# Optimization experiments

Measured on AMD Instinct MI355X. Metric: run time of the kernel, lower is better.

The kernel has to match this reference:

```python
import jax, jax.numpy as jnp
import numpy as np

N_HEAD = 16


def setup_inputs() -> dict:
    key = jax.random.key(0)
    k1, k2, k3 = jax.random.split(key, 3)
    B, T, N = 4, 2048, 1024
    x = jax.random.normal(k1, (B, T, N), dtype=jnp.float32)
    W_attn = jax.random.normal(k2, (N, 3 * N), dtype=jnp.float32) * (1.0 / np.sqrt(N))
    b_attn = jnp.zeros((3 * N,), dtype=jnp.float32)
    W_proj = jax.random.normal(k3, (N, N), dtype=jnp.float32) * (1.0 / np.sqrt(N))
    b_proj = jnp.zeros((N,), dtype=jnp.float32)
    return {"x": x, "W_attn": W_attn, "b_attn": b_attn, "W_proj": W_proj, "b_proj": b_proj}


def reference(x, W_attn, b_attn, W_proj, b_proj):
    B, T, N = x.shape
    H = N_HEAD
    Dh = N // H
    qkv = x @ W_attn + b_attn                      # [B, T, 3N]
    q, k, v = jnp.split(qkv, 3, axis=2)
    # [B, H, T, Dh]
    q = q.reshape(B, T, H, Dh).transpose(0, 2, 1, 3)
    k = k.reshape(B, T, H, Dh).transpose(0, 2, 1, 3)
    v = v.reshape(B, T, H, Dh).transpose(0, 2, 1, 3)
    att = jnp.einsum('bhqd,bhkd->bhqk', q, k) / (Dh ** 0.5)
    mask = jnp.tril(jnp.ones((T, T), dtype=bool))
    att = jnp.where(mask[None, None], att, jnp.finfo(x.dtype).min)
    att = jax.nn.softmax(att, axis=-1)
    y = jnp.einsum('bhqk,bhkd->bhqd', att, v)      # [B, H, T, Dh]
    y = y.transpose(0, 2, 1, 3).reshape(B, T, N)
    return y @ W_proj + b_proj
```

## Files before the change

kernel.cpp:

```cpp
#include <hip/hip_runtime.h>
#include <hip/hip_bf16.h>


typedef __attribute__((ext_vector_type(8))) short short8;
typedef __attribute__((ext_vector_type(4))) float f32x4;
typedef __attribute__((ext_vector_type(16))) float f32x16;

#define MFMA16(a, b, c) __builtin_amdgcn_mfma_f32_16x16x32_bf16((a), (b), (c), 0, 0, 0)
#define MFMA32(a, b, c) __builtin_amdgcn_mfma_f32_32x32x16_bf16((a), (b), (c), 0, 0, 0)

#if defined(__has_builtin)
#if __has_builtin(__builtin_amdgcn_exp2f)
#define EXP2(x) __builtin_amdgcn_exp2f(x)
#endif
#endif
#ifndef EXP2
#define EXP2(x) exp2f(x)
#endif

__device__ __forceinline__ void gload_lds16(const void* g, void* l) {
  __builtin_amdgcn_global_load_lds(
      (const __attribute__((address_space(1))) unsigned int*)g,
      (__attribute__((address_space(3))) unsigned int*)l, 16, 0, 0);
}

__device__ __forceinline__ unsigned pack_bf16x2(float lo, float hi) {
  unsigned ulo = __float_as_uint(lo) + 0x8000u;
  unsigned uhi = __float_as_uint(hi) + 0x8000u;
  return __builtin_amdgcn_perm(uhi, ulo, 0x07060302u);
}

__device__ __forceinline__ unsigned short bf16u(float f) {
  return (unsigned short)((__float_as_uint(f) + 0x8000u) >> 16);
}

__global__ void prep_kernel(const float* __restrict__ x, unsigned* __restrict__ Xb,
                            const float* __restrict__ Wa, __hip_bfloat16* __restrict__ WaT,
                            const float* __restrict__ Wp, __hip_bfloat16* __restrict__ WpT) {
  __shared__ float tile[32][33];
  const int tid = threadIdx.x;
  int blk = blockIdx.x;
  if (blk >= 4096) {
    int i = (blk - 4096) * 256 + tid;
    float4 v = ((const float4*)x)[i];
    uint2 o;
    o.x = pack_bf16x2(v.x, v.y);
    o.y = pack_bf16x2(v.z, v.w);
    ((uint2*)Xb)[i] = o;
    return;
  }
  const float* src;
  __hip_bfloat16* dst;
  int R, C, bx, by;
  if (blk < 3072) {
    src = Wa; dst = WaT; R = 1024; C = 3072; bx = blk % 96; by = blk / 96;
  } else {
    blk -= 3072;
    src = Wp; dst = WpT; R = 1024; C = 1024; bx = blk & 31; by = blk >> 5;
  }
  const int tx = tid & 31, ty = tid >> 5;
  const int c0 = bx * 32, r0 = by * 32;
#pragma unroll
  for (int i = 0; i < 32; i += 8)
    tile[ty + i][tx] = src[(long)(r0 + ty + i) * C + c0 + tx];
  __syncthreads();
#pragma unroll
  for (int i = 0; i < 32; i += 8)
    dst[(long)(c0 + ty + i) * R + r0 + tx] = __float2bfloat16(tile[tx][ty + i]);
}

template <int EPI>
__global__ __launch_bounds__(256, 2) void gemm_bt(
    const __hip_bfloat16* __restrict__ A, const __hip_bfloat16* __restrict__ Bt,
    const float* __restrict__ bias, void* o0, void* o1, void* o2, int N, int K) {
  __shared__ alignas(16) char smem[34816];
  short8 (*As)[8] = (short8(*)[8])smem;
  short8 (*Bs)[8] = (short8(*)[8])(smem + 16384);
  unsigned short (*C16)[136] = (unsigned short(*)[136])smem;
  float (*C32)[132] = (float(*)[132])smem;

  const int tid = threadIdx.x;
  const int lane = tid & 63, w = tid >> 6;
  const int l15 = lane & 15, quad = lane >> 4;
  const int wm = (w >> 1) * 64, wn = (w & 1) * 64;
  const int rowBase = blockIdx.y * 128;
  const int colBase = blockIdx.x * 128;
  const int sr8 = lane >> 3;
  const int scc = (lane & 7) ^ sr8;

  f32x4 acc[4][4];
#pragma unroll
  for (int mi = 0; mi < 4; ++mi)
#pragma unroll
    for (int ni = 0; ni < 4; ++ni)
      acc[mi][ni] = {0.f, 0.f, 0.f, 0.f};

  for (int k0 = 0; k0 < K; k0 += 64) {
    __syncthreads();
#pragma unroll
    for (int p = 0; p < 4; ++p) {
      const int rb = p * 32 + w * 8;
      const int row = rb + sr8;
      gload_lds16(A + (rowBase + row) * K + k0 + scc * 8, &As[rb][0]);
      gload_lds16(Bt + (colBase + row) * K + k0 + scc * 8, &Bs[rb][0]);
    }
    __syncthreads();
#pragma unroll
    for (int kc = 0; kc < 2; ++kc) {
      short8 af[4], bf[4];
#pragma unroll
      for (int mi = 0; mi < 4; ++mi) {
        int row = wm + mi * 16 + l15;
        af[mi] = As[row][(kc * 4 + quad) ^ (row & 7)];
      }
#pragma unroll
      for (int ni = 0; ni < 4; ++ni) {
        int row = wn + ni * 16 + l15;
        bf[ni] = Bs[row][(kc * 4 + quad) ^ (row & 7)];
      }
#pragma unroll
      for (int mi = 0; mi < 4; ++mi)
#pragma unroll
        for (int ni = 0; ni < 4; ++ni)
          acc[mi][ni] = MFMA16(af[mi], bf[ni], acc[mi][ni]);
    }
  }

  float bcol[4];
#pragma unroll
  for (int ni = 0; ni < 4; ++ni) bcol[ni] = bias[colBase + wn + ni * 16 + l15];

  if (EPI == 0) {
    const int which = colBase >> 10;
    const int b = rowBase >> 11;
    const int tt0 = rowBase & 2047;
    const int n1base = colBase & 1023;
    const float osc = (which == 0) ? 0.180336880111f : 1.0f;
    __syncthreads();
    if (which != 2) {
#pragma unroll
      for (int mi = 0; mi < 4; ++mi)
#pragma unroll
        for (int ni = 0; ni < 4; ++ni)
#pragma unroll
          for (int r = 0; r < 4; ++r)
            C16[wm + mi * 16 + quad * 4 + r][wn + ni * 16 + l15] =
                bf16u((acc[mi][ni][r] + bcol[ni]) * osc);
    } else {
#pragma unroll
      for (int mi = 0; mi < 4; ++mi)
#pragma unroll
        for (int ni = 0; ni < 4; ++ni)
#pragma unroll
          for (int r = 0; r < 4; ++r)
            C16[wn + ni * 16 + l15][wm + mi * 16 + quad * 4 + r] =
                bf16u(acc[mi][ni][r] + bcol[ni]);
    }
    __syncthreads();
    unsigned short* o = (unsigned short*)(which == 0 ? o0 : which == 1 ? o1 : o2);
    if (which != 2) {
#pragma unroll
      for (int j = 0; j < 8; ++j) {
        int flat = j * 256 + tid;
        int trow = flat >> 4, ch = flat & 15;
        int h = (n1base + ((ch & 8) << 3)) >> 6;
        long addr = ((long)((b * 16 + h) * 2048 + tt0 + trow)) * 64 + (ch & 7) * 8;
        *(short8*)&o[addr] = *(const short8*)&C16[trow][ch * 8];
      }
    } else {
#pragma unroll
      for (int j = 0; j < 8; ++j) {
        int flat = j * 256 + tid;
        int dcol = flat >> 4, ch = flat & 15;
        int h = (n1base + (dcol & 64)) >> 6;
        long addr = ((long)((b * 16 + h) * 64 + (dcol & 63))) * 2048 + tt0 + ch * 8;
        *(short8*)&o[addr] = *(const short8*)&C16[dcol][ch * 8];
      }
    }
  } else {
    float* out = (float*)o0;
    for (int p = 0; p < 2; ++p) {
      __syncthreads();
      if ((w >> 1) == p) {
#pragma unroll
        for (int mi = 0; mi < 4; ++mi)
#pragma unroll
          for (int ni = 0; ni < 4; ++ni)
#pragma unroll
            for (int r = 0; r < 4; ++r)
              C32[mi * 16 + quad * 4 + r][wn + ni * 16 + l15] =
                  acc[mi][ni][r] + bcol[ni];
      }
      __syncthreads();
#pragma unroll
      for (int j = 0; j < 8; ++j) {
        int flat = j * 256 + tid;
        int row = flat >> 5, ch = flat & 31;
        float4 v4 = *(const float4*)&C32[row][ch * 4];
        *(float4*)&out[(long)(rowBase + p * 64 + row) * N + colBase + ch * 4] = v4;
      }
    }
  }
}

__global__ __launch_bounds__(256, 4) void attn_kernel(
    const __hip_bfloat16* __restrict__ Q, const __hip_bfloat16* __restrict__ K,
    const __hip_bfloat16* __restrict__ Vt, __hip_bfloat16* __restrict__ Y, int T) {
  __shared__ short8 Ks[3][32][8];
  __shared__ short8 Vs[3][32][8];
  const int tid = threadIdx.x;
  const int w = tid >> 6, lane = tid & 63;
  const int c31 = lane & 31, half = lane >> 5;
  const int rsw = c31 & 7;
  const int idx = blockIdx.x;
  const int bh = idx & 63;
  const int b = bh >> 4, h = bh & 15;
  const int qsel = idx >> 6;
  const int qq = qsel >> 2, qp = qsel & 3;
  const int jt = (qq == 0) ? 15 - qp : (qq == 1) ? 8 + qp : (qq == 2) ? 4 + qp : 3 - qp;

  const int qrow0 = jt * 128 + w * 32;
  const __hip_bfloat16* Qp = Q + (long)bh * T * 64;
  const __hip_bfloat16* Kp = K + (long)bh * T * 64;
  const __hip_bfloat16* Vp = Vt + (long)bh * 64 * T;

  const int sr8 = lane >> 3;
  const int srow = w * 8 + sr8;
  const int scc = (lane & 7) ^ (srow & 7);
  const int vrow = srow + ((scc >> 2) << 5);
  const int vkoff = (scc & 3) * 8;

  short8 qf[4];
#pragma unroll
  for (int s = 0; s < 4; ++s)
    qf[s] = *(const short8*)(Qp + (qrow0 + c31) * 64 + s * 16 + half * 8);

  f32x16 czero;
#pragma unroll
  for (int i = 0; i < 16; ++i) czero[i] = 0.f;
  f32x16 oacc[2];
#pragma unroll
  for (int g = 0; g < 2; ++g) oacc[g] = czero;
  float lsum = 0.f;
  const int myq = qrow0 + c31;
  const int nkt = 4 * jt + 4;
  const int my_nkt = 4 * jt + w + 1;
  const int my_diag = my_nkt - 1;

#define STAGE_ATTN(buf, kbase)                                             \
  do {                                                                     \
    gload_lds16(Kp + ((kbase) + srow) * 64 + scc * 8, &Ks[buf][w * 8][0]); \
    gload_lds16(Vp + (long)vrow * T + (kbase) + vkoff, &Vs[buf][w * 8][0]);\
  } while (0)

  STAGE_ATTN(0, 0);
  STAGE_ATTN(1, 32);
  int bcur = 0;

  for (int kt = 0; kt < nkt; ++kt) {
    if (kt < nkt - 1)
      asm volatile("s_waitcnt vmcnt(2)" ::: "memory");
    else
      asm volatile("s_waitcnt vmcnt(0)" ::: "memory");
    __builtin_amdgcn_s_barrier();
    __builtin_amdgcn_sched_barrier(0);

    if (kt + 2 < nkt) {
      const int bs = (bcur >= 1) ? bcur - 1 : 2;
      STAGE_ATTN(bs, (kt + 2) * 32);
    }

    if (kt < my_nkt) {
      const int kb = kt * 32;
      short8 af[4];
#pragma unroll
      for (int s = 0; s < 4; ++s)
        af[s] = Ks[bcur][c31][(s * 2 + half) ^ rsw];
      __builtin_amdgcn_s_setprio(1);
      f32x16 z = MFMA32(af[0], qf[0], czero);
#pragma unroll
      for (int s = 1; s < 4; ++s) z = MFMA32(af[s], qf[s], z);
      __builtin_amdgcn_s_setprio(0);
      if (kt == my_diag) {
#pragma unroll
        for (int r = 0; r < 16; ++r) {
          int key = kb + (r & 3) + 8 * (r >> 2) + 4 * half;
          if (key > myq) z[r] = -INFINITY;
        }
      }
      unsigned pk[8];
#pragma unroll
      for (int i = 0; i < 8; ++i) {
        float p0 = EXP2(z[2 * i]);
        float p1 = EXP2(z[2 * i + 1]);
        lsum += p0 + p1;
        pk[i] = pack_bf16x2(p0, p1);
      }
      short8 pb[2];
#pragma unroll
      for (int s = 0; s < 2; ++s) {
        auto r0 = __builtin_amdgcn_permlane32_swap(pk[4 * s + 0], pk[4 * s + 2],
                                                   false, false);
        auto r1 = __builtin_amdgcn_permlane32_swap(pk[4 * s + 1], pk[4 * s + 3],
                                                   false, false);
        union { unsigned u[4]; short8 s8; } cv;
        cv.u[0] = r0[0]; cv.u[1] = r1[0]; cv.u[2] = r0[1]; cv.u[3] = r1[1];
        pb[s] = cv.s8;
      }
      short8 vf[2][2];
#pragma unroll
      for (int dg = 0; dg < 2; ++dg)
#pragma unroll
        for (int S = 0; S < 2; ++S)
          vf[dg][S] = Vs[bcur][c31][(dg * 4 + S * 2 + half) ^ rsw];
      __builtin_amdgcn_s_setprio(1);
#pragma unroll
      for (int dg = 0; dg < 2; ++dg)
#pragma unroll
        for (int S = 0; S < 2; ++S)
          oacc[dg] = MFMA32(vf[dg][S], pb[S], oacc[dg]);
      __builtin_amdgcn_s_setprio(0);
    }
    bcur = (bcur == 2) ? 0 : bcur + 1;
  }

  lsum += __shfl_xor(lsum, 32);

  const float inv = 1.0f / lsum;
  unsigned short* Yu = (unsigned short*)Y;
  const long rowoff = ((long)(b * 2048 + qrow0 + c31)) * 1024 + h * 64;
#pragma unroll
  for (int dg = 0; dg < 2; ++dg)
#pragma unroll
    for (int rg = 0; rg < 4; ++rg) {
      uint2 o;
      o.x = pack_bf16x2(oacc[dg][rg * 4 + 0] * inv, oacc[dg][rg * 4 + 1] * inv);
      o.y = pack_bf16x2(oacc[dg][rg * 4 + 2] * inv, oacc[dg][rg * 4 + 3] * inv);
      *(uint2*)&Yu[rowoff + dg * 32 + half * 4 + rg * 8] = o;
    }
}

extern "C" void kernel_launch(void* const* d_in, const int* in_sizes, int n_in,
                              void* d_out, int out_size, void* d_ws, size_t ws_size,
                              hipStream_t stream) {
  const float* x  = (const float*)d_in[0];
  const float* Wa = (const float*)d_in[1];
  const float* ba = (const float*)d_in[2];
  const float* Wp = (const float*)d_in[3];
  const float* bp = (const float*)d_in[4];
  float* out = (float*)d_out;

  char* ws = (char*)d_ws;
  __hip_bfloat16* Xb  = (__hip_bfloat16*)(ws);
  __hip_bfloat16* WaT = (__hip_bfloat16*)(ws + 16777216);
  __hip_bfloat16* WpT = (__hip_bfloat16*)(ws + 23068672);
  __hip_bfloat16* Qb  = (__hip_bfloat16*)(ws + 25165824);
  __hip_bfloat16* Kb  = (__hip_bfloat16*)(ws + 41943040);
  __hip_bfloat16* Vtb = (__hip_bfloat16*)(ws + 58720256);
  __hip_bfloat16* Yb  = (__hip_bfloat16*)(ws + 75497472);
  if (ws_size < 92274688) return;

  prep_kernel<<<12288, 256, 0, stream>>>(x, (unsigned*)Xb, Wa, WaT, Wp, WpT);
  gemm_bt<0><<<dim3(24, 64), 256, 0, stream>>>(Xb, WaT, ba, Qb, Kb, Vtb, 3072, 1024);
  attn_kernel<<<dim3(1024), dim3(256), 0, stream>>>(Qb, Kb, Vtb, Yb, 2048);
  gemm_bt<1><<<dim3(8, 64), 256, 0, stream>>>(Yb, WpT, bp, out, nullptr, nullptr, 1024, 1024);
}
```

Baseline: 226.5 us.

## Replace LDS-staged 4-wave attention blocks with single-wave blocks loading K/V from global

The attention kernel changes from 256-thread blocks, which share K and V tiles through a triple-buffered LDS pipeline with barriers, to 64-thread single-wave blocks that each own 32 query rows. Each wave loads its K and V fragments straight from global memory, and the grid grows to 4096 blocks with query tiles interleaved from both ends of the sequence for causal load balance. This removes block-wide barriers and LDS staging. In exchange, K/V reuse across waves now depends on the cache, and the loads are no longer prefetched ahead of use.

Result: slower. 352.0 us (+55.4%).

```diff
diff --git a/kernel.cpp b/kernel.cpp
--- a/kernel.cpp
+++ b/kernel.cpp
@@ -203,33 +203,22 @@
   }
 }
 
-__global__ __launch_bounds__(256, 4) void attn_kernel(
+__global__ __launch_bounds__(64, 4) void attn_kernel(
     const __hip_bfloat16* __restrict__ Q, const __hip_bfloat16* __restrict__ K,
     const __hip_bfloat16* __restrict__ Vt, __hip_bfloat16* __restrict__ Y, int T) {
-  __shared__ short8 Ks[3][32][8];
-  __shared__ short8 Vs[3][32][8];
-  const int tid = threadIdx.x;
-  const int w = tid >> 6, lane = tid & 63;
+  const int lane = threadIdx.x;
   const int c31 = lane & 31, half = lane >> 5;
-  const int rsw = c31 & 7;
   const int idx = blockIdx.x;
   const int bh = idx & 63;
   const int b = bh >> 4, h = bh & 15;
   const int qsel = idx >> 6;
-  const int qq = qsel >> 2, qp = qsel & 3;
-  const int jt = (qq == 0) ? 15 - qp : (qq == 1) ? 8 + qp : (qq == 2) ? 4 + qp : 3 - qp;
-
-  const int qrow0 = jt * 128 + w * 32;
+  const int jt = (qsel & 1) ? (qsel >> 1) : 63 - (qsel >> 1);
+
+  const int qrow0 = jt * 32;
   const __hip_bfloat16* Qp = Q + (long)bh * T * 64;
   const __hip_bfloat16* Kp = K + (long)bh * T * 64;
   const __hip_bfloat16* Vp = Vt + (long)bh * 64 * T;
 
-  const int sr8 = lane >> 3;
-  const int srow = w * 8 + sr8;
-  const int scc = (lane & 7) ^ (srow & 7);
-  const int vrow = srow + ((scc >> 2) << 5);
-  const int vkoff = (scc & 3) * 8;
-
   short8 qf[4];
 #pragma unroll
   for (int s = 0; s < 4; ++s)
@@ -243,85 +232,55 @@
   for (int g = 0; g < 2; ++g) oacc[g] = czero;
   float lsum = 0.f;
   const int myq = qrow0 + c31;
-  const int nkt = 4 * jt + 4;
-  const int my_nkt = 4 * jt + w + 1;
-  const int my_diag = my_nkt - 1;
-
-#define STAGE_ATTN(buf, kbase)                                             \
-  do {                                                                     \
-    gload_lds16(Kp + ((kbase) + srow) * 64 + scc * 8, &Ks[buf][w * 8][0]); \
-    gload_lds16(Vp + (long)vrow * T + (kbase) + vkoff, &Vs[buf][w * 8][0]);\
-  } while (0)
-
-  STAGE_ATTN(0, 0);
-  STAGE_ATTN(1, 32);
-  int bcur = 0;
+  const int nkt = jt + 1;
 
   for (int kt = 0; kt < nkt; ++kt) {
-    if (kt < nkt - 1)
-      asm volatile("s_waitcnt vmcnt(2)" ::: "memory");
-    else
-      asm volatile("s_waitcnt vmcnt(0)" ::: "memory");
-    __builtin_amdgcn_s_barrier();
-    __builtin_amdgcn_sched_barrier(0);
-
-    if (kt + 2 < nkt) {
-      const int bs = (bcur >= 1) ? bcur - 1 : 2;
-      STAGE_ATTN(bs, (kt + 2) * 32);
-    }
-
-    if (kt < my_nkt) {
-      const int kb = kt * 32;
-      short8 af[4];
-#pragma unroll
-      for (int s = 0; s < 4; ++s)
-        af[s] = Ks[bcur][c31][(s * 2 + half) ^ rsw];
-      __builtin_amdgcn_s_setprio(1);
-      f32x16 z = MFMA32(af[0], qf[0], czero);
-#pragma unroll
-      for (int s = 1; s < 4; ++s) z = MFMA32(af[s], qf[s], z);
-      __builtin_amdgcn_s_setprio(0);
-      if (kt == my_diag) {
-#pragma unroll
-        for (int r = 0; r < 16; ++r) {
-          int key = kb + (r & 3) + 8 * (r >> 2) + 4 * half;
-          if (key > myq) z[r] = -INFINITY;
-        }
-      }
-      unsigned pk[8];
-#pragma unroll
-      for (int i = 0; i < 8; ++i) {
-        float p0 = EXP2(z[2 * i]);
-        float p1 = EXP2(z[2 * i + 1]);
-        lsum += p0 + p1;
-        pk[i] = pack_bf16x2(p0, p1);
-      }
-      short8 pb[2];
-#pragma unroll
-      for (int s = 0; s < 2; ++s) {
-        auto r0 = __builtin_amdgcn_permlane32_swap(pk[4 * s + 0], pk[4 * s + 2],
-                                                   false, false);
-        auto r1 = __builtin_amdgcn_permlane32_swap(pk[4 * s + 1], pk[4 * s + 3],
-                                                   false, false);
-        union { unsigned u[4]; short8 s8; } cv;
-        cv.u[0] = r0[0]; cv.u[1] = r1[0]; cv.u[2] = r0[1]; cv.u[3] = r1[1];
-        pb[s] = cv.s8;
-      }
-      short8 vf[2][2];
-#pragma unroll
-      for (int dg = 0; dg < 2; ++dg)
-#pragma unroll
-        for (int S = 0; S < 2; ++S)
-          vf[dg][S] = Vs[bcur][c31][(dg * 4 + S * 2 + half) ^ rsw];
-      __builtin_amdgcn_s_setprio(1);
-#pragma unroll
-      for (int dg = 0; dg < 2; ++dg)
-#pragma unroll
-        for (int S = 0; S < 2; ++S)
-          oacc[dg] = MFMA32(vf[dg][S], pb[S], oacc[dg]);
-      __builtin_amdgcn_s_setprio(0);
-    }
-    bcur = (bcur == 2) ? 0 : bcur + 1;
+    const int kb = kt * 32;
+    short8 af[4];
+#pragma unroll
+    for (int s = 0; s < 4; ++s)
+      af[s] = *(const short8*)(Kp + (kb + c31) * 64 + s * 16 + half * 8);
+    short8 vf[2][2];
+#pragma unroll
+    for (int dg = 0; dg < 2; ++dg)
+#pragma unroll
+      for (int S = 0; S < 2; ++S)
+        vf[dg][S] = *(const short8*)(Vp + (long)(dg * 32 + c31) * T + kb +
+                                     S * 16 + half * 8);
+    f32x16 z = MFMA32(af[0], qf[0], czero);
+#pragma unroll
+    for (int s = 1; s < 4; ++s) z = MFMA32(af[s], qf[s], z);
+    if (kt == jt) {
+#pragma unroll
+      for (int r = 0; r < 16; ++r) {
+        int key = kb + (r & 3) + 8 * (r >> 2) + 4 * half;
+        if (key > myq) z[r] = -INFINITY;
+      }
+    }
+    unsigned pk[8];
+#pragma unroll
+    for (int i = 0; i < 8; ++i) {
+      float p0 = EXP2(z[2 * i]);
+      float p1 = EXP2(z[2 * i + 1]);
+      lsum += p0 + p1;
+      pk[i] = pack_bf16x2(p0, p1);
+    }
+    short8 pb[2];
+#pragma unroll
+    for (int s = 0; s < 2; ++s) {
+      auto r0 = __builtin_amdgcn_permlane32_swap(pk[4 * s + 0], pk[4 * s + 2],
+                                                 false, false);
+      auto r1 = __builtin_amdgcn_permlane32_swap(pk[4 * s + 1], pk[4 * s + 3],
+                                                 false, false);
+      union { unsigned u[4]; short8 s8; } cv;
+      cv.u[0] = r0[0]; cv.u[1] = r1[0]; cv.u[2] = r0[1]; cv.u[3] = r1[1];
+      pb[s] = cv.s8;
+    }
+#pragma unroll
+    for (int dg = 0; dg < 2; ++dg)
+#pragma unroll
+      for (int S = 0; S < 2; ++S)
+        oacc[dg] = MFMA32(vf[dg][S], pb[S], oacc[dg]);
   }
 
   lsum += __shfl_xor(lsum, 32);
@@ -362,6 +321,6 @@
 
   prep_kernel<<<12288, 256, 0, stream>>>(x, (unsigned*)Xb, Wa, WaT, Wp, WpT);
   gemm_bt<0><<<dim3(24, 64), 256, 0, stream>>>(Xb, WaT, ba, Qb, Kb, Vtb, 3072, 1024);
-  attn_kernel<<<dim3(1024), dim3(256), 0, stream>>>(Qb, Kb, Vtb, Yb, 2048);
+  attn_kernel<<<dim3(4096), dim3(64), 0, stream>>>(Qb, Kb, Vtb, Yb, 2048);
   gemm_bt<1><<<dim3(8, 64), 256, 0, stream>>>(Yb, WpT, bp, out, nullptr, nullptr, 1024, 1024);
 }
```
